# Kernel optimization log

Hardware: AMD Instinct MI355X
Metric: run time of the kernel (lower is better)

The kernel has to match this reference:

```python
import jax, jax.numpy as jnp
import numpy as np

LEAKY_ALPHA = 0.2  # LeakyReLU negative slope from init arg `alpha`


def setup_inputs() -> dict:
    key = jax.random.key(0)
    k1, k2, k3, k4 = jax.random.split(key, 4)
    B, N, Fin, Fout = 8, 2048, 256, 256
    h = jax.random.normal(k1, (B, N, Fin), dtype=jnp.float32)
    adj = jax.random.randint(k2, (N, N), 0, 2, dtype=jnp.int32)
    W = jax.random.normal(k3, (Fin, Fout), dtype=jnp.float32) * (1.414 * (6.0 / (Fin + Fout)) ** 0.5)
    a = jax.random.normal(k4, (2 * Fout, 1), dtype=jnp.float32) * (1.414 * (6.0 / (2 * Fout + 1)) ** 0.5)
    return {"h": h, "adj": adj, "W": W, "a": a}


def reference(h, adj, W, a):
    # h: (B, N, Fin), adj: (N, N) int {0,1}, W: (Fin, Fout), a: (2*Fout, 1)
    Fout = W.shape[1]
    Wh = jnp.einsum('bnf,fo->bno', h, W)            # (B, N, Fout)
    a1 = a[:Fout, 0]                                  # attends to target node i
    a2 = a[Fout:, 0]                                  # attends to source node j
    # a^T [Wh_i || Wh_j] == (Wh_i . a1) + (Wh_j . a2); LeakyReLU applied after, as in original
    s_i = Wh @ a1                                     # (B, N)
    s_j = Wh @ a2                                     # (B, N)
    e = jax.nn.leaky_relu(s_i[:, :, None] + s_j[:, None, :], negative_slope=LEAKY_ALPHA)  # (B, N, N)
    N = Wh.shape[1]
    mask = (adj > 0) | jnp.eye(N, dtype=bool)         # adjacency + self-loops
    e = jnp.where(mask[None, :, :], e, -jnp.inf)
    attention = jax.nn.softmax(e, axis=-1)            # dropout is identity in eval
    attention = jnp.nan_to_num(attention, nan=0.0)
    h_prime = jnp.einsum('bij,bjo->bio', attention, Wh)  # (B, N, Fout)
    return jax.nn.elu(h_prime)                        # concat=True -> ELU
```

## Files before the change

kernel.cpp:

```cpp
#include <hip/hip_runtime.h>

typedef unsigned short u16;
typedef unsigned int   u32;
typedef unsigned long long u64;

typedef __bf16 bf16x8 __attribute__((ext_vector_type(8)));
typedef float  f32x4  __attribute__((ext_vector_type(4)));

#define MFMA_BF16(a,b,c) __builtin_amdgcn_mfma_f32_16x16x32_bf16((a),(b),(c),0,0,0)

__device__ __forceinline__ float bf2f(u16 u) {
    return __uint_as_float(((u32)u) << 16);
}
__device__ __forceinline__ u16 f2bf(float x) {
    u32 u = __float_as_uint(x);
    u += 0x7fffu + ((u >> 16) & 1u);
    return (u16)(u >> 16);
}
__device__ __forceinline__ float ldany(const void* p, size_t i, int f32) {
    return f32 ? ((const float*)p)[i] : bf2f(((const u16*)p)[i]);
}
__device__ __forceinline__ int detect_f32(const u32* hw) {
    u32 w = hw[threadIdx.x & 63];
    int e = (w >> 23) & 0xFF;
    u64 m = __ballot(e >= 64 && e <= 190);
    return __popcll(m) >= 32 ? 1 : 0;
}

__global__ __launch_bounds__(256) void kprep0(const void* __restrict__ w, const void* __restrict__ a,
                                              u16* __restrict__ wt, float* __restrict__ wa1,
                                              float* __restrict__ wa2, int* __restrict__ cnt,
                                              const u32* __restrict__ hw) {
    __shared__ float s1[4], s2[4];
    int bid = blockIdx.x, t = threadIdx.x;
    int wid = t >> 6, lane = t & 63;
    if (bid == 0 && t < 8) cnt[t] = 0;
    int f32 = detect_f32(hw);
    int k = bid, o = t;
    float wv = ldany(w, (size_t)k * 256 + o, f32);
    wt[o * 256 + k] = f2bf(wv);
    float p1 = wv * ldany(a, o, f32);
    float p2 = wv * ldany(a, 256 + o, f32);
    for (int d = 32; d; d >>= 1) { p1 += __shfl_down(p1, d); p2 += __shfl_down(p2, d); }
    if (lane == 0) { s1[wid] = p1; s2[wid] = p2; }
    __syncthreads();
    if (o == 0) { wa1[k] = s1[0] + s1[1] + s1[2] + s1[3]; wa2[k] = s2[0] + s2[1] + s2[2] + s2[3]; }
}

struct __align__(16) K2LDS {
    u16 At[64 * 68];
    union { u16 Bt[256 * 68]; u16 Ct[256 * 68]; };
    float wa1s[256], wa2s[256];
    float s1[64], s2[64];
};
__global__ __launch_bounds__(1024, 4) void k2m(const void* __restrict__ h, const u16* __restrict__ wt,
                                               const float* __restrict__ wa1, const float* __restrict__ wa2,
                                               u16* __restrict__ whbt,
                                               float* __restrict__ sig, float* __restrict__ sjg,
                                               const int* __restrict__ adj, u64* __restrict__ mb64) {
    __shared__ K2LDS L;
    int bid = blockIdx.x;
    int t = threadIdx.x;
    int wid = t >> 6, lane = t & 63, ln = lane & 15, qd = lane >> 4;

    if (bid >= 256) {
        int w2 = (bid - 256) * 16 + wid;
        int4 v[8];
        #pragma unroll
        for (int s = 0; s < 8; s++) {
            int task = w2 * 8 + s;
            int row = task >> 3, jb = (task & 7) * 256;
            v[s] = *(const int4*)(adj + (size_t)row * 2048 + jb + lane * 4);
        }
        #pragma unroll
        for (int s = 0; s < 8; s++) {
            int task = w2 * 8 + s;
            int row = task >> 3, jb = (task & 7) * 256;
            int j0 = jb + lane * 4;
            u32 nib = (u32)(v[s].x > 0 || j0     == row)
                    | ((u32)(v[s].y > 0 || j0 + 1 == row) << 1)
                    | ((u32)(v[s].z > 0 || j0 + 2 == row) << 2)
                    | ((u32)(v[s].w > 0 || j0 + 3 == row) << 3);
            u32 sh = 4 * (lane & 7);
            u32 lo = (lane & 8) ? 0u : (nib << sh);
            u32 hi = (lane & 8) ? (nib << sh) : 0u;
            #pragma unroll
            for (int d = 1; d <= 8; d <<= 1) {
                lo |= __shfl_xor(lo, d);
                hi |= __shfl_xor(hi, d);
            }
            if ((lane & 15) == 0)
                mb64[(size_t)row * 32 + (jb >> 6) + (lane >> 4)] =
                    (u64)lo | ((u64)hi << 32);
        }
        return;
    }

    int f32 = detect_f32((const u32*)h);
    int m0 = bid * 64;
    int b  = m0 >> 11;
    int n0 = m0 & 2047;

    if (t < 256) { L.wa1s[t] = wa1[t]; L.wa2s[t] = wa2[t]; }
    if (t < 64) { L.s1[t] = 0.f; L.s2[t] = 0.f; }
    __syncthreads();

    float a1 = 0.f, a2 = 0.f;
    f32x4 acc[4];
    for (int mi = 0; mi < 4; mi++) acc[mi] = (f32x4){0.f, 0.f, 0.f, 0.f};

    for (int c = 0; c < 4; c++) {
        int k0c = c * 64;
        if (t < 512) {
            int r = t >> 3, s = t & 7;
            float xv[8]; u16 uv[8];
            if (f32) {
                const float* src = (const float*)h + (size_t)(m0 + r) * 256 + k0c + s * 8;
                f32x4 x0 = *(const f32x4*)src;
                f32x4 x1 = *(const f32x4*)(src + 4);
                #pragma unroll
                for (int q = 0; q < 4; q++) { xv[q] = x0[q]; xv[4 + q] = x1[q]; }
                #pragma unroll
                for (int q = 0; q < 8; q++) uv[q] = f2bf(xv[q]);
            } else {
                const u16* src = (const u16*)h + (size_t)(m0 + r) * 256 + k0c + s * 8;
                *(uint4*)uv = *(const uint4*)src;
                #pragma unroll
                for (int q = 0; q < 8; q++) xv[q] = bf2f(uv[q]);
            }
            *(uint4*)&L.At[r * 68 + s * 8] = *(uint4*)uv;
            float pa = 0.f, pb = 0.f;
            #pragma unroll
            for (int q = 0; q < 8; q++) {
                pa += xv[q] * L.wa1s[k0c + s * 8 + q];
                pb += xv[q] * L.wa2s[k0c + s * 8 + q];
            }
            a1 += pa; a2 += pb;
        } else {
            int tt = t - 512;
            #pragma unroll
            for (int p = 0; p < 4; p++) {
                int f = (tt >> 3) + p * 64, s = tt & 7;
                *(uint4*)&L.Bt[f * 68 + s * 8] =
                    *(const uint4*)(wt + (size_t)f * 256 + k0c + s * 8);
            }
        }
        __syncthreads();
        for (int ks = 0; ks < 2; ks++) {
            bf16x8 af[4], bfr;
            for (int mi = 0; mi < 4; mi++)
                af[mi] = *(const bf16x8*)&L.At[(mi * 16 + ln) * 68 + ks * 32 + qd * 8];
            bfr = *(const bf16x8*)&L.Bt[(wid * 16 + ln) * 68 + ks * 32 + qd * 8];
            for (int mi = 0; mi < 4; mi++)
                acc[mi] = MFMA_BF16(af[mi], bfr, acc[mi]);
        }
        __syncthreads();
    }

    if (t < 512) {
        atomicAdd(&L.s1[t >> 3], a1);
        atomicAdd(&L.s2[t >> 3], a2);
    }
    for (int mi = 0; mi < 4; mi++) {
        int f = wid * 16 + ln;
        int n = mi * 16 + qd * 4;
        u16 v[4];
        for (int r = 0; r < 4; r++) v[r] = f2bf(acc[mi][r]);
        *(uint2*)&L.Ct[f * 68 + n] = *(uint2*)v;
    }
    __syncthreads();
    if (t < 64) { sig[m0 + t] = L.s1[t]; sjg[m0 + t] = L.s2[t]; }
    {
        int fr = t >> 2, q0 = (t & 3) * 2;
        size_t base = (size_t)b * 524288 + (size_t)fr * 2048 + n0;
        #pragma unroll
        for (int k = 0; k < 2; k++) {
            int s = q0 + k;
            uint4 v = *(uint4*)&L.Ct[fr * 68 + s * 8];
            *(uint4*)(whbt + base + s * 8) = v;
        }
    }
}

struct __align__(16) K4LDS {
    u32   vpack[2048];
    u16   sjb[2048];
    u64   mw[64 * 33];
    float u1[64], u2[64], nsi[64], inv[64];
    float lred[1024];
    u16   Pt[2][8192];
    int   claim[2];
};
__global__ __launch_bounds__(1024, 4) void k4(const float* __restrict__ sig,
                                              const float* __restrict__ sjg,
                                              const u64* __restrict__ mb64, const u16* __restrict__ whbt,
                                              void* __restrict__ out, const void* __restrict__ hdet,
                                              int* __restrict__ cnt) {
    __shared__ K4LDS L;
    int f32 = detect_f32((const u32*)hdet);
    int t = threadIdx.x;
    if (t == 0) {
        int xcd = __builtin_amdgcn_s_getreg(63508) & 7;
        int bsel = 0, tile = 0;
        #pragma unroll
        for (int k = 0; k < 8; k++) {
            int bb = (xcd + k) & 7;
            int tt = atomicAdd(&cnt[bb], 1);
            if (tt < 32) { bsel = bb; tile = tt; break; }
        }
        L.claim[0] = bsel; L.claim[1] = tile;
    }
    __syncthreads();
    int b  = L.claim[0];
    int i0 = L.claim[1] * 64;
    int wid = t >> 6, lane = t & 63, ln = lane & 15, qd = lane >> 4;
    const u16* wb = whbt + (size_t)b * 524288 + (size_t)wid * 16 * 2048;
    float lacc = 0.f;

    bf16x8 br[2][4];
    #define LOAD_B(cc, bb) do {                                             \
        int j0_ = (cc) * 128;                                               \
        _Pragma("unroll")                                                   \
        for (int ks = 0; ks < 4; ks++)                                      \
            br[bb][ks] = *(const bf16x8*)(wb +                              \
                (size_t)ln * 2048 + j0_ + ks * 32 + qd * 8);                \
    } while (0)

    #define PGEN(cc, bb) do {                                               \
        int r_ = t & 63, o_ = t >> 6;                                       \
        int jb_ = (cc) * 128 + o_ * 8;                                      \
        uint4 pkA_ = *(const uint4*)&L.vpack[jb_];                          \
        uint4 pkB_ = *(const uint4*)&L.vpack[jb_ + 4];                      \
        uint4 sj4_ = *(const uint4*)&L.sjb[jb_];                            \
        u32 mb_ = (u32)(L.mw[r_ * 33 + 2 * (cc) + (o_ >> 3)]                \
                        >> ((o_ & 7) * 8)) & 0xffu;                         \
        float u1_ = L.u1[r_], u2_ = L.u2[r_], nsi_ = L.nsi[r_];             \
        u32 pr_[4];                                                         \
        _Pragma("unroll")                                                   \
        for (int pk = 0; pk < 4; pk++) {                                    \
            u32 vw0_ = (pk == 0) ? pkA_.x : (pk == 1) ? pkA_.z              \
                     : (pk == 2) ? pkB_.x : pkB_.z;                         \
            u32 vw1_ = (pk == 0) ? pkA_.y : (pk == 1) ? pkA_.w              \
                     : (pk == 2) ? pkB_.y : pkB_.w;                         \
            u32 sw_ = (pk == 0) ? sj4_.x : (pk == 1) ? sj4_.y               \
                     : (pk == 2) ? sj4_.z : sj4_.w;                         \
            float sj0_ = __uint_as_float(sw_ << 16);                        \
            float sj1_ = __uint_as_float(sw_ & 0xffff0000u);                \
            float p0_, p1_;                                                 \
            {                                                               \
                bool pos = sj0_ > nsi_;                                     \
                float vv = __uint_as_float(pos ? (vw0_ << 16)               \
                                               : ((vw0_ >> 16) << 16));     \
                p0_ = (pos ? u1_ : u2_) * vv;                               \
                p0_ = ((mb_ >> (2 * pk)) & 1u) ? p0_ : 0.f;                 \
            }                                                               \
            {                                                               \
                bool pos = sj1_ > nsi_;                                     \
                float vv = __uint_as_float(pos ? (vw1_ << 16)               \
                                               : ((vw1_ >> 16) << 16));     \
                p1_ = (pos ? u1_ : u2_) * vv;                               \
                p1_ = ((mb_ >> (2 * pk + 1)) & 1u) ? p1_ : 0.f;             \
            }                                                               \
            lacc += p0_ + p1_;                                              \
            pr_[pk] = __builtin_amdgcn_perm(__float_as_uint(p1_),           \
                                            __float_as_uint(p0_),           \
                                            0x07060302u);                   \
        }                                                                   \
        *(uint4*)&L.Pt[bb][t * 8] = *(uint4*)pr_;                           \
    } while (0)

    LOAD_B(0, 0);
    float sjv0 = sjg[b * 2048 + t];
    float sjv1 = sjg[b * 2048 + 1024 + t];
    {
        float mx = fmaxf(sjv0, sjv1);
        for (int d = 32; d; d >>= 1) mx = fmaxf(mx, __shfl_xor(mx, d));
        if (lane == 0) L.lred[wid] = mx;
    }
    for (int p = 0; p < 2; p++) {
        int idx = t + p * 1024;
        int r = idx >> 5, c = idx & 31;
        L.mw[r * 33 + c] = mb64[(size_t)(i0 + r) * 32 + c];
    }
    __syncthreads();
    float Mb;
    {
        float m0_ = fmaxf(fmaxf(fmaxf(L.lred[0], L.lred[1]), fmaxf(L.lred[2], L.lred[3])),
                          fmaxf(fmaxf(L.lred[4], L.lred[5]), fmaxf(L.lred[6], L.lred[7])));
        float m1_ = fmaxf(fmaxf(fmaxf(L.lred[8], L.lred[9]), fmaxf(L.lred[10], L.lred[11])),
                          fmaxf(fmaxf(L.lred[12], L.lred[13]), fmaxf(L.lred[14], L.lred[15])));
        Mb = fmaxf(m0_, m1_);
    }
    {
        float vj0 = __expf(sjv0 - Mb), v2j0 = __expf(0.2f * (sjv0 - Mb));
        L.vpack[t] = (u32)f2bf(vj0) | ((u32)f2bf(v2j0) << 16);
        L.sjb[t] = f2bf(sjv0);
        float vj1 = __expf(sjv1 - Mb), v2j1 = __expf(0.2f * (sjv1 - Mb));
        L.vpack[t + 1024] = (u32)f2bf(vj1) | ((u32)f2bf(v2j1) << 16);
        L.sjb[t + 1024] = f2bf(sjv1);
    }
    if (t < 64) {
        float siv = sig[b * 2048 + i0 + t];
        float x = siv + Mb;
        float K = fmaxf(x, 0.2f * x);
        L.u1[t] = __expf(x - K);
        L.u2[t] = __expf(0.2f * x - K);
        L.nsi[t] = -siv;
    }
    __syncthreads();
    PGEN(0, 0);

    f32x4 acc[4];
    for (int mi = 0; mi < 4; mi++)
        acc[mi] = (f32x4){0.f, 0.f, 0.f, 0.f};

    #define STEP(c, cur, nxt) do {                                          \
        __syncthreads();                                                    \
        if ((c) < 15) { LOAD_B((c) + 1, nxt); PGEN((c) + 1, nxt); }         \
        __builtin_amdgcn_s_setprio(1);                                      \
        _Pragma("unroll")                                                   \
        for (int ks = 0; ks < 4; ks++) {                                    \
            bf16x8 af[4];                                                   \
            _Pragma("unroll")                                               \
            for (int mi = 0; mi < 4; mi++)                                  \
                af[mi] = *(const bf16x8*)&L.Pt[cur][((ks * 4 + qd) * 64 +   \
                                                     mi * 16 + ln) * 8];    \
            _Pragma("unroll")                                               \
            for (int mi = 0; mi < 4; mi++)                                  \
                acc[mi] = MFMA_BF16(af[mi], br[cur][ks], acc[mi]);          \
        }                                                                   \
        __builtin_amdgcn_s_setprio(0);                                      \
    } while (0)

    for (int cc = 0; cc < 8; cc++) {
        STEP(2 * cc,     0, 1);
        STEP(2 * cc + 1, 1, 0);
    }

    __syncthreads();
    L.lred[t] = lacc;
    __syncthreads();
    if (t < 64) {
        float s = 0.f;
        #pragma unroll
        for (int q = 0; q < 16; q++) s += L.lred[q * 64 + t];
        L.inv[t] = 1.0f / s;
    }
    __syncthreads();

    {
        int fg = wid * 16 + ln;
        for (int mi = 0; mi < 4; mi++) {
            for (int reg = 0; reg < 4; reg++) {
                int rl = mi * 16 + qd * 4 + reg;
                float hp = acc[mi][reg] * L.inv[rl];
                float y = hp > 0.f ? hp : (__expf(hp) - 1.f);
                size_t idx = (size_t)(b * 2048 + i0 + rl) * 256 + fg;
                if (f32) ((float*)out)[idx] = y;
                else     ((u16*)out)[idx]   = f2bf(y);
            }
        }
    }
    #undef LOAD_B
    #undef PGEN
    #undef STEP
}

extern "C" void kernel_launch(void* const* d_in, const int* in_sizes, int n_in,
                              void* d_out, int out_size, void* d_ws, size_t ws_size,
                              hipStream_t stream) {
    const void* h   = d_in[0];
    const int*  adj = (const int*)d_in[1];
    const void* W   = d_in[2];
    const void* a   = d_in[3];

    char* ws = (char*)d_ws;
    u16*   WT    = (u16*)  (ws + 0);
    float* si    = (float*)(ws + 131072);
    float* sj    = (float*)(ws + 196608);
    u64*   mb64  = (u64*)  (ws + 557056);
    u16*   whbt  = (u16*)  (ws + 1081344);
    float* Wa1   = (float*)(ws + 9469952);
    float* Wa2   = (float*)(ws + 9470976);
    int*   cnt   = (int*)  (ws + 9472000);

    kprep0<<<dim3(256), dim3(256),  0, stream>>>(W, a, WT, Wa1, Wa2, cnt, (const u32*)h);
    k2m   <<<dim3(384), dim3(1024), 0, stream>>>(h, WT, Wa1, Wa2, whbt, si, sj, adj, mb64);
    k4    <<<dim3(256), dim3(1024), 0, stream>>>(si, sj, mb64, whbt, d_out, h, cnt);
}
```

Baseline: 131.0 us.

## Prefetch next K-chunk into registers in projection GEMM and use lighter barriers

The projection kernel's K loop now issues the global loads for chunk c+1 into registers before staging and computing chunk c, so global latency overlaps the MFMA work. Barriers in that loop and in the attention STEP loop are replaced by a custom barrier that waits only on LDS/scalar counters (lgkmcnt) and not on outstanding vector memory loads, which lets prefetches stay in flight across the barrier. This raises register pressure, and it relies on the compiler inserting waits before the prefetched registers are consumed.

```diff
diff --git a/kernel.cpp b/kernel.cpp
--- a/kernel.cpp
+++ b/kernel.cpp
@@ -25,6 +25,10 @@
     int e = (w >> 23) & 0xFF;
     u64 m = __ballot(e >= 64 && e <= 190);
     return __popcll(m) >= 32 ? 1 : 0;
+}
+__device__ __forceinline__ void lbar() {
+    asm volatile("s_waitcnt lgkmcnt(0)" ::: "memory");
+    __builtin_amdgcn_s_barrier();
 }
 
 __global__ __launch_bounds__(256) void kprep0(const void* __restrict__ w, const void* __restrict__ a,
@@ -109,43 +113,76 @@
     f32x4 acc[4];
     for (int mi = 0; mi < 4; mi++) acc[mi] = (f32x4){0.f, 0.f, 0.f, 0.f};
 
+    uint4 c0 = {}, c1 = {}, c2 = {}, c3 = {};
+    uint4 n0r = {}, n1r = {}, n2r = {}, n3r = {};
+
+    #define LDH(cc, R0, R1) do {                                            \
+        int r_ = t >> 3, s_ = t & 7;                                        \
+        if (f32) {                                                          \
+            const uint4* src_ = (const uint4*)((const float*)h +            \
+                (size_t)(m0 + r_) * 256 + (cc) * 64 + s_ * 8);              \
+            R0 = src_[0]; R1 = src_[1];                                     \
+        } else {                                                            \
+            R0 = *(const uint4*)((const u16*)h +                            \
+                (size_t)(m0 + r_) * 256 + (cc) * 64 + s_ * 8);              \
+        }                                                                   \
+    } while (0)
+
+    #define STAGE_A(cc, R0, R1) do {                                        \
+        int r_ = t >> 3, s_ = t & 7;                                        \
+        float xv_[8]; u16 uv_[8];                                           \
+        if (f32) {                                                          \
+            u32 w0_[4], w1_[4];                                             \
+            *(uint4*)w0_ = R0; *(uint4*)w1_ = R1;                           \
+            _Pragma("unroll")                                               \
+            for (int q = 0; q < 4; q++) {                                   \
+                xv_[q]     = __uint_as_float(w0_[q]);                       \
+                xv_[4 + q] = __uint_as_float(w1_[q]);                       \
+            }                                                               \
+            _Pragma("unroll")                                               \
+            for (int q = 0; q < 8; q++) uv_[q] = f2bf(xv_[q]);              \
+        } else {                                                            \
+            *(uint4*)uv_ = R0;                                              \
+            _Pragma("unroll")                                               \
+            for (int q = 0; q < 8; q++) xv_[q] = bf2f(uv_[q]);              \
+        }                                                                   \
+        *(uint4*)&L.At[r_ * 68 + s_ * 8] = *(uint4*)uv_;                    \
+        float pa_ = 0.f, pb_ = 0.f;                                         \
+        _Pragma("unroll")                                                   \
+        for (int q = 0; q < 8; q++) {                                       \
+            pa_ += xv_[q] * L.wa1s[(cc) * 64 + s_ * 8 + q];                 \
+            pb_ += xv_[q] * L.wa2s[(cc) * 64 + s_ * 8 + q];                 \
+        }                                                                   \
+        a1 += pa_; a2 += pb_;                                               \
+    } while (0)
+
+    #define LDW(cc, W0, W1, W2, W3) do {                                    \
+        int tt_ = t - 512, s_ = tt_ & 7, f_ = tt_ >> 3;                     \
+        W0 = *(const uint4*)(wt + (size_t)(f_      ) * 256 + (cc) * 64 + s_ * 8); \
+        W1 = *(const uint4*)(wt + (size_t)(f_ +  64) * 256 + (cc) * 64 + s_ * 8); \
+        W2 = *(const uint4*)(wt + (size_t)(f_ + 128) * 256 + (cc) * 64 + s_ * 8); \
+        W3 = *(const uint4*)(wt + (size_t)(f_ + 192) * 256 + (cc) * 64 + s_ * 8); \
+    } while (0)
+
+    #define STAGE_B(W0, W1, W2, W3) do {                                    \
+        int tt_ = t - 512, s_ = tt_ & 7, f_ = tt_ >> 3;                     \
+        *(uint4*)&L.Bt[(f_      ) * 68 + s_ * 8] = W0;                      \
+        *(uint4*)&L.Bt[(f_ +  64) * 68 + s_ * 8] = W1;                      \
+        *(uint4*)&L.Bt[(f_ + 128) * 68 + s_ * 8] = W2;                      \
+        *(uint4*)&L.Bt[(f_ + 192) * 68 + s_ * 8] = W3;                      \
+    } while (0)
+
+    if (t < 512) LDH(0, c0, c1); else LDW(0, c0, c1, c2, c3);
+
+    #pragma unroll
     for (int c = 0; c < 4; c++) {
-        int k0c = c * 64;
-        if (t < 512) {
-            int r = t >> 3, s = t & 7;
-            float xv[8]; u16 uv[8];
-            if (f32) {
-                const float* src = (const float*)h + (size_t)(m0 + r) * 256 + k0c + s * 8;
-                f32x4 x0 = *(const f32x4*)src;
-                f32x4 x1 = *(const f32x4*)(src + 4);
-                #pragma unroll
-                for (int q = 0; q < 4; q++) { xv[q] = x0[q]; xv[4 + q] = x1[q]; }
-                #pragma unroll
-                for (int q = 0; q < 8; q++) uv[q] = f2bf(xv[q]);
-            } else {
-                const u16* src = (const u16*)h + (size_t)(m0 + r) * 256 + k0c + s * 8;
-                *(uint4*)uv = *(const uint4*)src;
-                #pragma unroll
-                for (int q = 0; q < 8; q++) xv[q] = bf2f(uv[q]);
-            }
-            *(uint4*)&L.At[r * 68 + s * 8] = *(uint4*)uv;
-            float pa = 0.f, pb = 0.f;
-            #pragma unroll
-            for (int q = 0; q < 8; q++) {
-                pa += xv[q] * L.wa1s[k0c + s * 8 + q];
-                pb += xv[q] * L.wa2s[k0c + s * 8 + q];
-            }
-            a1 += pa; a2 += pb;
-        } else {
-            int tt = t - 512;
-            #pragma unroll
-            for (int p = 0; p < 4; p++) {
-                int f = (tt >> 3) + p * 64, s = tt & 7;
-                *(uint4*)&L.Bt[f * 68 + s * 8] =
-                    *(const uint4*)(wt + (size_t)f * 256 + k0c + s * 8);
-            }
-        }
-        __syncthreads();
+        if (c < 3) {
+            if (t < 512) LDH(c + 1, n0r, n1r);
+            else         LDW(c + 1, n0r, n1r, n2r, n3r);
+        }
+        if (t < 512) STAGE_A(c, c0, c1);
+        else         STAGE_B(c0, c1, c2, c3);
+        lbar();
         for (int ks = 0; ks < 2; ks++) {
             bf16x8 af[4], bfr;
             for (int mi = 0; mi < 4; mi++)
@@ -154,8 +191,13 @@
             for (int mi = 0; mi < 4; mi++)
                 acc[mi] = MFMA_BF16(af[mi], bfr, acc[mi]);
         }
-        __syncthreads();
-    }
+        lbar();
+        if (c < 3) { c0 = n0r; c1 = n1r; c2 = n2r; c3 = n3r; }
+    }
+    #undef LDH
+    #undef STAGE_A
+    #undef LDW
+    #undef STAGE_B
 
     if (t < 512) {
         atomicAdd(&L.s1[t >> 3], a1);
@@ -315,7 +357,7 @@
         acc[mi] = (f32x4){0.f, 0.f, 0.f, 0.f};
 
     #define STEP(c, cur, nxt) do {                                          \
-        __syncthreads();                                                    \
+        lbar();                                                             \
         if ((c) < 15) { LOAD_B((c) + 1, nxt); PGEN((c) + 1, nxt); }         \
         __builtin_amdgcn_s_setprio(1);                                      \
         _Pragma("unroll")                                                   \
```

After: 133.8 us. 1.02x slower.

## Switch attention-aggregation GEMM to 32x32x16 MFMA with 2x8 wave tiling

Applied to the files above, without the earlier changes.

Replaces the 16x16x32 MFMA tiling (each wave owning 16 feature columns across all 64 rows) with 32x32x16 MFMA, where each wave owns a 32x32 output tile (2 row groups by 8 feature groups). This cuts the A-fragment LDS reads per MFMA and doubles the B register buffer. The __syncthreads is replaced by a manual lgkmcnt wait plus s_barrier. A large LDS padding array is added, which raises LDS use and likely lowers how many blocks fit per CU. That may be deliberate, to limit occupancy.

```diff
diff --git a/kernel.cpp b/kernel.cpp
--- a/kernel.cpp
+++ b/kernel.cpp
@@ -6,8 +6,10 @@
 
 typedef __bf16 bf16x8 __attribute__((ext_vector_type(8)));
 typedef float  f32x4  __attribute__((ext_vector_type(4)));
-
-#define MFMA_BF16(a,b,c) __builtin_amdgcn_mfma_f32_16x16x32_bf16((a),(b),(c),0,0,0)
+typedef float  f32x16 __attribute__((ext_vector_type(16)));
+
+#define MFMA_BF16(a,b,c)   __builtin_amdgcn_mfma_f32_16x16x32_bf16((a),(b),(c),0,0,0)
+#define MFMA32_BF16(a,b,c) __builtin_amdgcn_mfma_f32_32x32x16_bf16((a),(b),(c),0,0,0)
 
 __device__ __forceinline__ float bf2f(u16 u) {
     return __uint_as_float(((u32)u) << 16);
@@ -25,6 +27,10 @@
     int e = (w >> 23) & 0xFF;
     u64 m = __ballot(e >= 64 && e <= 190);
     return __popcll(m) >= 32 ? 1 : 0;
+}
+__device__ __forceinline__ void lbar() {
+    asm volatile("s_waitcnt lgkmcnt(0)" ::: "memory");
+    __builtin_amdgcn_s_barrier();
 }
 
 __global__ __launch_bounds__(256) void kprep0(const void* __restrict__ w, const void* __restrict__ a,
@@ -190,6 +196,7 @@
     float lred[1024];
     u16   Pt[2][8192];
     int   claim[2];
+    u32   pad1blk[4096];
 };
 __global__ __launch_bounds__(1024, 4) void k4(const float* __restrict__ sig,
                                               const float* __restrict__ sjg,
@@ -213,17 +220,19 @@
     __syncthreads();
     int b  = L.claim[0];
     int i0 = L.claim[1] * 64;
-    int wid = t >> 6, lane = t & 63, ln = lane & 15, qd = lane >> 4;
-    const u16* wb = whbt + (size_t)b * 524288 + (size_t)wid * 16 * 2048;
+    int wid = t >> 6, lane = t & 63;
+    int l31 = lane & 31, h5 = lane >> 5;
+    int fg = wid & 7, ig = wid >> 3;
+    const u16* wb = whbt + (size_t)b * 524288 + (size_t)fg * 32 * 2048;
     float lacc = 0.f;
 
-    bf16x8 br[2][4];
+    bf16x8 br[2][8];
     #define LOAD_B(cc, bb) do {                                             \
         int j0_ = (cc) * 128;                                               \
         _Pragma("unroll")                                                   \
-        for (int ks = 0; ks < 4; ks++)                                      \
+        for (int ks = 0; ks < 8; ks++)                                      \
             br[bb][ks] = *(const bf16x8*)(wb +                              \
-                (size_t)ln * 2048 + j0_ + ks * 32 + qd * 8);                \
+                (size_t)l31 * 2048 + j0_ + ks * 16 + h5 * 8);               \
     } while (0)
 
     #define PGEN(cc, bb) do {                                               \
@@ -310,24 +319,19 @@
     __syncthreads();
     PGEN(0, 0);
 
-    f32x4 acc[4];
-    for (int mi = 0; mi < 4; mi++)
-        acc[mi] = (f32x4){0.f, 0.f, 0.f, 0.f};
+    f32x16 acc;
+    #pragma unroll
+    for (int q = 0; q < 16; q++) acc[q] = 0.f;
 
     #define STEP(c, cur, nxt) do {                                          \
-        __syncthreads();                                                    \
+        lbar();                                                             \
         if ((c) < 15) { LOAD_B((c) + 1, nxt); PGEN((c) + 1, nxt); }         \
         __builtin_amdgcn_s_setprio(1);                                      \
         _Pragma("unroll")                                                   \
-        for (int ks = 0; ks < 4; ks++) {                                    \
-            bf16x8 af[4];                                                   \
-            _Pragma("unroll")                                               \
-            for (int mi = 0; mi < 4; mi++)                                  \
-                af[mi] = *(const bf16x8*)&L.Pt[cur][((ks * 4 + qd) * 64 +   \
-                                                     mi * 16 + ln) * 8];    \
-            _Pragma("unroll")                                               \
-            for (int mi = 0; mi < 4; mi++)                                  \
-                acc[mi] = MFMA_BF16(af[mi], br[cur][ks], acc[mi]);          \
+        for (int ks = 0; ks < 8; ks++) {                                    \
+            bf16x8 af = *(const bf16x8*)&L.Pt[cur][((ks * 2 + h5) * 64 +    \
+                                                    ig * 32 + l31) * 8];    \
+            acc = MFMA32_BF16(af, br[cur][ks], acc);                        \
         }                                                                   \
         __builtin_amdgcn_s_setprio(0);                                      \
     } while (0)
@@ -349,16 +353,15 @@
     __syncthreads();
 
     {
-        int fg = wid * 16 + ln;
-        for (int mi = 0; mi < 4; mi++) {
-            for (int reg = 0; reg < 4; reg++) {
-                int rl = mi * 16 + qd * 4 + reg;
-                float hp = acc[mi][reg] * L.inv[rl];
-                float y = hp > 0.f ? hp : (__expf(hp) - 1.f);
-                size_t idx = (size_t)(b * 2048 + i0 + rl) * 256 + fg;
-                if (f32) ((float*)out)[idx] = y;
-                else     ((u16*)out)[idx]   = f2bf(y);
-            }
+        int fcol = fg * 32 + l31;
+        #pragma unroll
+        for (int reg = 0; reg < 16; reg++) {
+            int il = ig * 32 + (reg & 3) + 8 * (reg >> 2) + 4 * h5;
+            float hp = acc[reg] * L.inv[il];
+            float y = hp > 0.f ? hp : (__expf(hp) - 1.f);
+            size_t idx = (size_t)(b * 2048 + i0 + il) * 256 + fcol;
+            if (f32) ((float*)out)[idx] = y;
+            else     ((u16*)out)[idx]   = f2bf(y);
         }
     }
     #undef LOAD_B
```

After: 161.2 us. 23.1% more time.

## Split attention-aggregation tiles into 32 rows by half the features for more blocks

Applied to the files above, without the earlier changes.

The aggregation kernel now uses 512-thread blocks, each covering 32 query rows and 128 of the 256 output features, launched as 1024 blocks instead of 256. The aim is to fill more CUs and improve latency hiding on a GPU with more compute units than the old block count. In exchange, the softmax probability generation (exp/mask work) is done twice per row tile, once for each feature half, and the j-side precompute per block is the same size as before, so redundant work grows.

```diff
diff --git a/kernel.cpp b/kernel.cpp
--- a/kernel.cpp
+++ b/kernel.cpp
@@ -185,17 +185,17 @@
 struct __align__(16) K4LDS {
     u32   vpack[2048];
     u16   sjb[2048];
-    u64   mw[64 * 33];
-    float u1[64], u2[64], nsi[64], inv[64];
-    float lred[1024];
-    u16   Pt[2][8192];
+    u64   mw[32 * 33];
+    float u1[32], u2[32], nsi[32], inv[32];
+    float lred[512];
+    u16   Pt[2][4096];
     int   claim[2];
 };
-__global__ __launch_bounds__(1024, 4) void k4(const float* __restrict__ sig,
-                                              const float* __restrict__ sjg,
-                                              const u64* __restrict__ mb64, const u16* __restrict__ whbt,
-                                              void* __restrict__ out, const void* __restrict__ hdet,
-                                              int* __restrict__ cnt) {
+__global__ __launch_bounds__(512, 8) void k4(const float* __restrict__ sig,
+                                             const float* __restrict__ sjg,
+                                             const u64* __restrict__ mb64, const u16* __restrict__ whbt,
+                                             void* __restrict__ out, const void* __restrict__ hdet,
+                                             int* __restrict__ cnt) {
     __shared__ K4LDS L;
     int f32 = detect_f32((const u32*)hdet);
     int t = threadIdx.x;
@@ -206,15 +206,17 @@
         for (int k = 0; k < 8; k++) {
             int bb = (xcd + k) & 7;
             int tt = atomicAdd(&cnt[bb], 1);
-            if (tt < 32) { bsel = bb; tile = tt; break; }
+            if (tt < 128) { bsel = bb; tile = tt; break; }
         }
         L.claim[0] = bsel; L.claim[1] = tile;
     }
     __syncthreads();
-    int b  = L.claim[0];
-    int i0 = L.claim[1] * 64;
+    int b    = L.claim[0];
+    int tile = L.claim[1];
+    int i0 = (tile >> 1) * 32;
+    int fh = tile & 1;
     int wid = t >> 6, lane = t & 63, ln = lane & 15, qd = lane >> 4;
-    const u16* wb = whbt + (size_t)b * 524288 + (size_t)wid * 16 * 2048;
+    const u16* wb = whbt + (size_t)b * 524288 + (size_t)(fh * 128 + wid * 16) * 2048;
     float lacc = 0.f;
 
     bf16x8 br[2][4];
@@ -227,7 +229,7 @@
     } while (0)
 
     #define PGEN(cc, bb) do {                                               \
-        int r_ = t & 63, o_ = t >> 6;                                       \
+        int r_ = t & 31, o_ = t >> 5;                                       \
         int jb_ = (cc) * 128 + o_ * 8;                                      \
         uint4 pkA_ = *(const uint4*)&L.vpack[jb_];                          \
         uint4 pkB_ = *(const uint4*)&L.vpack[jb_ + 4];                      \
@@ -270,36 +272,33 @@
     } while (0)
 
     LOAD_B(0, 0);
-    float sjv0 = sjg[b * 2048 + t];
-    float sjv1 = sjg[b * 2048 + 1024 + t];
+    float sjv[4];
+    #pragma unroll
+    for (int p = 0; p < 4; p++) sjv[p] = sjg[b * 2048 + t + p * 512];
     {
-        float mx = fmaxf(sjv0, sjv1);
+        float mx = fmaxf(fmaxf(sjv[0], sjv[1]), fmaxf(sjv[2], sjv[3]));
         for (int d = 32; d; d >>= 1) mx = fmaxf(mx, __shfl_xor(mx, d));
         if (lane == 0) L.lred[wid] = mx;
     }
     for (int p = 0; p < 2; p++) {
-        int idx = t + p * 1024;
+        int idx = t + p * 512;
         int r = idx >> 5, c = idx & 31;
         L.mw[r * 33 + c] = mb64[(size_t)(i0 + r) * 32 + c];
     }
     __syncthreads();
     float Mb;
     {
-        float m0_ = fmaxf(fmaxf(fmaxf(L.lred[0], L.lred[1]), fmaxf(L.lred[2], L.lred[3])),
-                          fmaxf(fmaxf(L.lred[4], L.lred[5]), fmaxf(L.lred[6], L.lred[7])));
-        float m1_ = fmaxf(fmaxf(fmaxf(L.lred[8], L.lred[9]), fmaxf(L.lred[10], L.lred[11])),
-                          fmaxf(fmaxf(L.lred[12], L.lred[13]), fmaxf(L.lred[14], L.lred[15])));
-        Mb = fmaxf(m0_, m1_);
-    }
-    {
-        float vj0 = __expf(sjv0 - Mb), v2j0 = __expf(0.2f * (sjv0 - Mb));
-        L.vpack[t] = (u32)f2bf(vj0) | ((u32)f2bf(v2j0) << 16);
-        L.sjb[t] = f2bf(sjv0);
-        float vj1 = __expf(sjv1 - Mb), v2j1 = __expf(0.2f * (sjv1 - Mb));
-        L.vpack[t + 1024] = (u32)f2bf(vj1) | ((u32)f2bf(v2j1) << 16);
-        L.sjb[t + 1024] = f2bf(sjv1);
-    }
-    if (t < 64) {
+        Mb = fmaxf(fmaxf(fmaxf(L.lred[0], L.lred[1]), fmaxf(L.lred[2], L.lred[3])),
+                   fmaxf(fmaxf(L.lred[4], L.lred[5]), fmaxf(L.lred[6], L.lred[7])));
+    }
+    #pragma unroll
+    for (int p = 0; p < 4; p++) {
+        int j = t + p * 512;
+        float vj = __expf(sjv[p] - Mb), v2j = __expf(0.2f * (sjv[p] - Mb));
+        L.vpack[j] = (u32)f2bf(vj) | ((u32)f2bf(v2j) << 16);
+        L.sjb[j] = f2bf(sjv[p]);
+    }
+    if (t < 32) {
         float siv = sig[b * 2048 + i0 + t];
         float x = siv + Mb;
         float K = fmaxf(x, 0.2f * x);
@@ -310,8 +309,8 @@
     __syncthreads();
     PGEN(0, 0);
 
-    f32x4 acc[4];
-    for (int mi = 0; mi < 4; mi++)
+    f32x4 acc[2];
+    for (int mi = 0; mi < 2; mi++)
         acc[mi] = (f32x4){0.f, 0.f, 0.f, 0.f};
 
     #define STEP(c, cur, nxt) do {                                          \
@@ -320,13 +319,13 @@
         __builtin_amdgcn_s_setprio(1);                                      \
         _Pragma("unroll")                                                   \
         for (int ks = 0; ks < 4; ks++) {                                    \
-            bf16x8 af[4];                                                   \
+            bf16x8 af[2];                                                   \
             _Pragma("unroll")                                               \
-            for (int mi = 0; mi < 4; mi++)                                  \
-                af[mi] = *(const bf16x8*)&L.Pt[cur][((ks * 4 + qd) * 64 +   \
+            for (int mi = 0; mi < 2; mi++)                                  \
+                af[mi] = *(const bf16x8*)&L.Pt[cur][((ks * 4 + qd) * 32 +   \
                                                      mi * 16 + ln) * 8];    \
             _Pragma("unroll")                                               \
-            for (int mi = 0; mi < 4; mi++)                                  \
+            for (int mi = 0; mi < 2; mi++)                                  \
                 acc[mi] = MFMA_BF16(af[mi], br[cur][ks], acc[mi]);          \
         }                                                                   \
         __builtin_amdgcn_s_setprio(0);                                      \
@@ -340,17 +339,17 @@
     __syncthreads();
     L.lred[t] = lacc;
     __syncthreads();
-    if (t < 64) {
+    if (t < 32) {
         float s = 0.f;
         #pragma unroll
-        for (int q = 0; q < 16; q++) s += L.lred[q * 64 + t];
+        for (int q = 0; q < 16; q++) s += L.lred[q * 32 + t];
         L.inv[t] = 1.0f / s;
     }
     __syncthreads();
 
     {
-        int fg = wid * 16 + ln;
-        for (int mi = 0; mi < 4; mi++) {
+        int fg = fh * 128 + wid * 16 + ln;
+        for (int mi = 0; mi < 2; mi++) {
             for (int reg = 0; reg < 4; reg++) {
                 int rl = mi * 16 + qd * 4 + reg;
                 float hp = acc[mi][reg] * L.inv[rl];
@@ -384,7 +383,7 @@
     float* Wa2   = (float*)(ws + 9470976);
     int*   cnt   = (int*)  (ws + 9472000);
 
-    kprep0<<<dim3(256), dim3(256),  0, stream>>>(W, a, WT, Wa1, Wa2, cnt, (const u32*)h);
-    k2m   <<<dim3(384), dim3(1024), 0, stream>>>(h, WT, Wa1, Wa2, whbt, si, sj, adj, mb64);
-    k4    <<<dim3(256), dim3(1024), 0, stream>>>(si, sj, mb64, whbt, d_out, h, cnt);
-}
+    kprep0<<<dim3(256),  dim3(256),  0, stream>>>(W, a, WT, Wa1, Wa2, cnt, (const u32*)h);
+    k2m   <<<dim3(384),  dim3(1024), 0, stream>>>(h, WT, Wa1, Wa2, whbt, si, sj, adj, mb64);
+    k4    <<<dim3(1024), dim3(512),  0, stream>>>(si, sj, mb64, whbt, d_out, h, cnt);
+}
```

Result: slower. 203.9 us (+55.7%).
